# Optimization experiments

Hardware: AMD Instinct MI355X
Metric: run time of the kernel (lower is better)

Reference implementation:

```python
import jax, jax.numpy as jnp
import numpy as np

N_HEADS = 32
EPS = 1e-7
ROPE_BASE = 10000.0


def rms_norm(x, gamma):
    return x / jnp.sqrt(EPS + jnp.mean(x * x, axis=-1, keepdims=True)) * gamma


def rope_tables(seq_len, head_dim, dtype=jnp.float32):
    inv_freq = 1.0 / (ROPE_BASE ** (jnp.arange(0, head_dim, 2, dtype=jnp.float32) / head_dim))
    angles = jnp.arange(seq_len, dtype=jnp.float32)[:, None] * inv_freq[None, :]  # [S, D/2]
    angles = jnp.concatenate([angles, angles], axis=-1)  # [S, D]
    return jnp.cos(angles).astype(dtype), jnp.sin(angles).astype(dtype)


def apply_rope(x, cos, sin):
    # x: [B, H, S, D]; cos/sin: [S, D]
    d = x.shape[-1]
    x1, x2 = x[..., : d // 2], x[..., d // 2 :]
    rotated = jnp.concatenate([-x2, x1], axis=-1)
    return x * cos[None, None] + rotated * sin[None, None]


def setup_inputs() -> dict:
    key = jax.random.key(0)
    ks = jax.random.split(key, 9)
    B, S, D, Hd = 1, 2048, 4096, 11008
    s = lambda k, shape, fan: jax.random.normal(k, shape, jnp.float32) * (fan ** -0.5)
    return {
        "X": jax.random.normal(ks[0], (B, S, D), jnp.float32),
        "Wq": s(ks[1], (D, D), D),
        "Wk": s(ks[2], (D, D), D),
        "Wv": s(ks[3], (D, D), D),
        "Wo": s(ks[4], (D, D), D),
        "bo": jnp.zeros((D,), jnp.float32),
        "gamma1": jnp.ones((D,), jnp.float32),
        "gamma2": jnp.ones((D,), jnp.float32),
        "W1": s(ks[5], (D, Hd), D),
        "W2": s(ks[6], (D, Hd), D),
        "W3": s(ks[7], (Hd, D), Hd),
    }


def reference(X, Wq, Wk, Wv, Wo, bo, gamma1, gamma2, W1, W2, W3):
    B, S, D = X.shape
    H = N_HEADS
    hd = D // H

    # --- attention sublayer ---
    h = rms_norm(X, gamma1)
    q = (h @ Wq).reshape(B, S, H, hd).transpose(0, 2, 1, 3)  # [B,H,S,hd]
    k = (h @ Wk).reshape(B, S, H, hd).transpose(0, 2, 1, 3)
    v = (h @ Wv).reshape(B, S, H, hd).transpose(0, 2, 1, 3)

    cos, sin = rope_tables(S, hd, X.dtype)
    q = apply_rope(q, cos, sin)
    k = apply_rope(k, cos, sin)

    scores = jnp.einsum("bhsd,bhtd->bhst", q, k) / jnp.sqrt(jnp.asarray(hd, X.dtype))
    causal = jnp.tril(jnp.ones((S, S), bool))
    scores = jnp.where(causal, scores, -jnp.inf)
    attn = jax.nn.softmax(scores, axis=-1)
    out = jnp.einsum("bhst,bhtd->bhsd", attn, v)
    out = out.transpose(0, 2, 1, 3).reshape(B, S, D)
    out = out @ Wo + bo
    X = X + out

    # --- SwiGLU FFN sublayer ---
    h2 = rms_norm(X, gamma2)
    x1 = h2 @ W1
    x2 = h2 @ W2
    ff = (x1 * jax.nn.sigmoid(x1) * x2) @ W3
    return X + ff
```

## Files before the change

kernel.cpp:

```cpp
#include <hip/hip_runtime.h>
#include <hip/hip_bf16.h>
#include <cstdint>
#include <cmath>

typedef __bf16 bf16;
typedef __attribute__((ext_vector_type(8))) __bf16 bf16x8;
typedef __attribute__((ext_vector_type(4))) __bf16 bf16x4;
typedef __attribute__((ext_vector_type(4))) float f32x4;

__device__ __forceinline__ void gload_lds16(const void* g, void* l) {
  __builtin_amdgcn_global_load_lds((__attribute__((address_space(1))) void*)g,
                                   (__attribute__((address_space(3))) void*)l,
                                   16, 0, 0);
}

template<int BM, int EPI>
__global__ __launch_bounds__(512, 2) void gemmd(
    const bf16* __restrict__ A, const bf16* __restrict__ Bt, void* __restrict__ Cv,
    const float* __restrict__ bias, const float* __restrict__ resid,
    const float* __restrict__ cosT, const float* __restrict__ sinT,
    bf16* __restrict__ q_out, bf16* __restrict__ k_out, bf16* __restrict__ v_out,
    int M, int N, int K, int gm) {
  extern __shared__ char lds[];
  constexpr int ASZ = BM * 128;
  constexpr int BUFS = ASZ + 32768;
  constexpr int MF = BM / 64;
  constexpr int LA = BM / 64;

  const int tid = threadIdx.x;
  const int wave = tid >> 6, lane = tid & 63;
  const int wr = wave >> 1, wc = wave & 1;
  const int l15 = lane & 15, l4 = lane >> 4;
  const int qq = gridDim.x >> 3;
  const int wgid = (blockIdx.x & 7) * qq + (blockIdx.x >> 3);
  const int tm = wgid % gm, tn = wgid / gm;
  const long brow = (long)tm * BM, bcol = (long)tn * 256;
  const int NT = K >> 6;
  const bf16* Ab = A + brow * K;
  const bf16* Bb = Bt + bcol * K;

  f32x4 acc[MF][8];
  #pragma unroll
  for (int i = 0; i < MF; ++i)
    #pragma unroll
    for (int j = 0; j < 8; ++j) acc[i][j] = (f32x4){0.f, 0.f, 0.f, 0.f};

  bf16x8 a[MF][2], b[8][2];

  auto stage = [&](int T) {
    const long kofs = (long)T << 6;
    char* wb = lds + (T & 1) * BUFS;
    #pragma unroll
    for (int i = 0; i < LA; ++i) {
      const int slot = i * 512 + tid, r = slot >> 3, c0 = slot & 7;
      gload_lds16(Ab + (long)r * K + kofs + ((c0 ^ (r & 7)) << 3), wb + slot * 16);
    }
    #pragma unroll
    for (int i = 0; i < 4; ++i) {
      const int slot = i * 512 + tid, r = slot >> 3, c0 = slot & 7;
      gload_lds16(Bb + (long)r * K + kofs + ((c0 ^ (r & 7)) << 3), wb + ASZ + slot * 16);
    }
  };

  stage(0);
  __syncthreads();

  for (int g = 0; g < NT; ++g) {
    const int pg = (g & 1) * BUFS;
    if (g + 1 < NT) stage(g + 1);
    #pragma unroll
    for (int nf = 0; nf < 8; ++nf)
      #pragma unroll
      for (int ks = 0; ks < 2; ++ks) {
        const int r = wc * 128 + nf * 16 + l15;
        b[nf][ks] = *(const bf16x8*)(lds + pg + ASZ + r * 128 + (((ks * 4 + l4) ^ (r & 7)) << 4));
      }
    #pragma unroll
    for (int mf = 0; mf < MF; ++mf)
      #pragma unroll
      for (int ks = 0; ks < 2; ++ks) {
        const int r = wr * (BM / 4) + mf * 16 + l15;
        a[mf][ks] = *(const bf16x8*)(lds + pg + r * 128 + (((ks * 4 + l4) ^ (r & 7)) << 4));
      }
    __builtin_amdgcn_s_setprio(1);
    #pragma unroll
    for (int ks = 0; ks < 2; ++ks)
      #pragma unroll
      for (int mf = 0; mf < MF; ++mf)
        #pragma unroll
        for (int nf = 0; nf < 8; ++nf)
          acc[mf][nf] = __builtin_amdgcn_mfma_f32_16x16x32_bf16(
              a[mf][ks], b[nf][ks], acc[mf][nf], 0, 0, 0);
    __builtin_amdgcn_s_setprio(0);
    __syncthreads();
  }

  if (EPI == 1 || EPI == 2) {
    #pragma unroll
    for (int mf = 0; mf < MF; ++mf) {
      const long row0 = brow + wr * (BM / 4) + mf * 16 + l4 * 4;
      #pragma unroll
      for (int nf = 0; nf < 8; ++nf) {
        const long col = bcol + wc * 128 + nf * 16 + l15;
        #pragma unroll
        for (int rj = 0; rj < 4; ++rj) {
          const long idx = (row0 + rj) * N + col;
          const float v = acc[mf][nf][rj];
          if (EPI == 1) ((float*)Cv)[idx] = v + bias[col] + resid[idx];
          else          ((float*)Cv)[idx] = v + resid[idx];
        }
      }
    }
  } else if (EPI == 3) {
    const int region = (int)(bcol >> 12);
    const int hc = (int)(bcol & 4095) + wc * 128;
    const int h = hc >> 7;
    if (region < 2) {
      bf16* dh = (region == 0 ? q_out : k_out) + (long)h * 2048 * 128;
      #pragma unroll
      for (int mf = 0; mf < MF; ++mf) {
        #pragma unroll
        for (int rj = 0; rj < 4; ++rj) {
          const int s = (int)brow + wr * (BM / 4) + mf * 16 + l4 * 4 + rj;
          const float* cr = cosT + s * 64;
          const float* sr = sinT + s * 64;
          #pragma unroll
          for (int nfp = 0; nfp < 4; ++nfp) {
            const int d = nfp * 16 + l15;
            const float c = cr[d], sn = sr[d];
            const float x1 = acc[mf][nfp][rj], x2 = acc[mf][nfp + 4][rj];
            dh[(long)s * 128 + d]      = (bf16)(x1 * c - x2 * sn);
            dh[(long)s * 128 + d + 64] = (bf16)(x2 * c + x1 * sn);
          }
        }
      }
    } else {
      bf16* dh = v_out + (long)h * 128 * 2048;
      #pragma unroll
      for (int mf = 0; mf < MF; ++mf) {
        const int s0 = (int)brow + wr * (BM / 4) + mf * 16 + l4 * 4;
        #pragma unroll
        for (int nf = 0; nf < 8; ++nf) {
          const int d = nf * 16 + l15;
          bf16x4 v;
          #pragma unroll
          for (int rj = 0; rj < 4; ++rj) v[rj] = (bf16)acc[mf][nf][rj];
          *(bf16x4*)(dh + (long)d * 2048 + s0) = v;
        }
      }
    }
  } else {
    #pragma unroll
    for (int mf = 0; mf < MF; ++mf) {
      #pragma unroll
      for (int rj = 0; rj < 4; ++rj) {
        const int s = (int)brow + wr * (BM / 4) + mf * 16 + l4 * 4 + rj;
        bf16* gr = (bf16*)Cv + (long)s * 11008;
        #pragma unroll
        for (int nfp = 0; nfp < 4; ++nfp) {
          const int col = (int)bcol + wc * 128 + nfp * 32 + l15;
          const int j = ((col >> 5) << 4) + l15;
          const float x1 = acc[mf][2 * nfp][rj], x2 = acc[mf][2 * nfp + 1][rj];
          const float sg = x1 / (1.f + __expf(-x1));
          gr[j] = (bf16)(sg * x2);
        }
      }
    }
  }
}

__global__ __launch_bounds__(256) void rmsnorm_kernel(
    const float* __restrict__ X, const float* __restrict__ gamma,
    bf16* __restrict__ out, int D) {
  const int row = blockIdx.x;
  const float* xr = X + (long)row * D;
  float ss = 0.f;
  for (int i = threadIdx.x * 4; i < D; i += 1024) {
    float4 v = *(const float4*)(xr + i);
    ss += v.x * v.x + v.y * v.y + v.z * v.z + v.w * v.w;
  }
  #pragma unroll
  for (int off = 32; off; off >>= 1) ss += __shfl_down(ss, off, 64);
  __shared__ float wsum[4];
  if ((threadIdx.x & 63) == 0) wsum[threadIdx.x >> 6] = ss;
  __syncthreads();
  const float tot = wsum[0] + wsum[1] + wsum[2] + wsum[3];
  const float scale = rsqrtf(1e-7f + tot / (float)D);
  bf16* orow = out + (long)row * D;
  for (int i = threadIdx.x * 4; i < D; i += 1024) {
    float4 v = *(const float4*)(xr + i);
    float4 g = *(const float4*)(gamma + i);
    orow[i]     = (bf16)(v.x * scale * g.x);
    orow[i + 1] = (bf16)(v.y * scale * g.y);
    orow[i + 2] = (bf16)(v.z * scale * g.z);
    orow[i + 3] = (bf16)(v.w * scale * g.w);
  }
}

__global__ __launch_bounds__(256) void wtrans_kernel(
    const float* __restrict__ in, bf16* __restrict__ out, int R, int C) {
  __shared__ float t[64][65];
  const int bx = blockIdx.x, by = blockIdx.y;
  const int lr = threadIdx.x >> 4;
  const int lc4 = (threadIdx.x & 15) * 4;
  #pragma unroll
  for (int i = 0; i < 4; ++i) {
    const int r = lr + i * 16;
    const float4 v = *(const float4*)(in + (long)(by * 64 + r) * C + bx * 64 + lc4);
    t[r][lc4] = v.x; t[r][lc4 + 1] = v.y; t[r][lc4 + 2] = v.z; t[r][lc4 + 3] = v.w;
  }
  __syncthreads();
  const int oc = threadIdx.x >> 4;
  const int or4 = (threadIdx.x & 15) * 4;
  #pragma unroll
  for (int i = 0; i < 4; ++i) {
    const int c = oc + i * 16;
    bf16x4 v;
    #pragma unroll
    for (int j = 0; j < 4; ++j) v[j] = (bf16)t[or4 + j][c];
    *(bf16x4*)(out + (long)(bx * 64 + c) * R + by * 64 + or4) = v;
  }
}

__global__ __launch_bounds__(256) void w12trans_kernel(
    const float* __restrict__ in, bf16* __restrict__ out, int off) {
  __shared__ float t[64][65];
  const int bx = blockIdx.x, by = blockIdx.y;
  const int lk = threadIdx.x >> 4;
  const int lj4 = (threadIdx.x & 15) * 4;
  #pragma unroll
  for (int i = 0; i < 4; ++i) {
    const int k = lk + i * 16;
    const float4 v = *(const float4*)(in + (long)(by * 64 + k) * 11008 + bx * 64 + lj4);
    t[k][lj4] = v.x; t[k][lj4 + 1] = v.y; t[k][lj4 + 2] = v.z; t[k][lj4 + 3] = v.w;
  }
  __syncthreads();
  const int oj = threadIdx.x >> 4;
  const int ok4 = (threadIdx.x & 15) * 4;
  #pragma unroll
  for (int i = 0; i < 4; ++i) {
    const int j = bx * 64 + oj + i * 16;
    const int r = ((j >> 4) << 5) + off + (j & 15);
    bf16x4 v;
    #pragma unroll
    for (int jj = 0; jj < 4; ++jj) v[jj] = (bf16)t[ok4 + jj][oj + i * 16];
    *(bf16x4*)(out + (long)r * 4096 + by * 64 + ok4) = v;
  }
}

__global__ __launch_bounds__(256) void rope_table_kernel(float* __restrict__ cosT,
                                                         float* __restrict__ sinT) {
  const int idx = blockIdx.x * 256 + threadIdx.x;
  const int i = idx & 63, s = idx >> 6;
  const float inv = powf(10000.f, -(float)i / 64.f);
  const float ang = (float)s * inv;
  cosT[idx] = cosf(ang);
  sinT[idx] = sinf(ang);
}

__global__ __launch_bounds__(256) void attn_kernel(
    const bf16* __restrict__ qh, const bf16* __restrict__ kh,
    const bf16* __restrict__ vt, bf16* __restrict__ outb) {
  constexpr int S = 2048;
  const int qb = blockIdx.x, head = blockIdx.y;
  const int tid = threadIdx.x, wave = tid >> 6, lane = tid & 63;
  __shared__ bf16 Ks[64 * 128];
  __shared__ bf16 Vs[128 * 64];
  __shared__ bf16 Plds[4][16 * 64];
  const bf16* qhh = qh + (long)head * S * 128;
  const bf16* khh = kh + (long)head * S * 128;
  const bf16* vth = vt + (long)head * 128 * S;

  const int l15 = lane & 15, l4 = lane >> 4;
  const int qrow = qb * 64 + wave * 16 + l15;
  bf16x8 qf[4];
  #pragma unroll
  for (int kf = 0; kf < 4; ++kf)
    qf[kf] = *(const bf16x8*)(qhh + (long)qrow * 128 + kf * 32 + l4 * 8);

  float m_r[4], l_r[4];
  #pragma unroll
  for (int r = 0; r < 4; ++r) { m_r[r] = -INFINITY; l_r[r] = 0.f; }
  f32x4 oacc[8] = {};
  const float scale = 0.08838834764831845f;

  for (int tb = 0; tb <= qb; ++tb) {
    #pragma unroll
    for (int i = 0; i < 4; ++i) {
      const int c = wave + 4 * i;
      gload_lds16(khh + (long)(tb * 64 + c * 4 + l4) * 128 + l15 * 8, Ks + c * 512);
      gload_lds16(vth + (long)(c * 8 + (lane >> 3)) * S + tb * 64 + (lane & 7) * 8, Vs + c * 512);
    }
    __syncthreads();

    f32x4 sf[4];
    #pragma unroll
    for (int ft = 0; ft < 4; ++ft) {
      f32x4 acn = {};
      #pragma unroll
      for (int kf = 0; kf < 4; ++kf) {
        bf16x8 kfr = *(const bf16x8*)(Ks + (ft * 16 + l15) * 128 + kf * 32 + l4 * 8);
        acn = __builtin_amdgcn_mfma_f32_16x16x32_bf16(qf[kf], kfr, acn, 0, 0, 0);
      }
      #pragma unroll
      for (int r = 0; r < 4; ++r) sf[ft][r] = acn[r] * scale;
    }
    if (tb == qb) {
      #pragma unroll
      for (int ft = 0; ft < 4; ++ft) {
        const int t_l = ft * 16 + l15;
        #pragma unroll
        for (int r = 0; r < 4; ++r)
          if (t_l > wave * 16 + l4 * 4 + r) sf[ft][r] = -INFINITY;
      }
    }
    float scl[4];
    #pragma unroll
    for (int r = 0; r < 4; ++r) {
      float mx = fmaxf(fmaxf(sf[0][r], sf[1][r]), fmaxf(sf[2][r], sf[3][r]));
      mx = fmaxf(mx, __shfl_xor(mx, 1, 64));
      mx = fmaxf(mx, __shfl_xor(mx, 2, 64));
      mx = fmaxf(mx, __shfl_xor(mx, 4, 64));
      mx = fmaxf(mx, __shfl_xor(mx, 8, 64));
      const float mnew = fmaxf(m_r[r], mx);
      scl[r] = __expf(m_r[r] - mnew);
      m_r[r] = mnew;
      float rs = 0.f;
      #pragma unroll
      for (int ft = 0; ft < 4; ++ft) {
        const float pexp = __expf(sf[ft][r] - mnew);
        sf[ft][r] = pexp;
        rs += pexp;
      }
      rs += __shfl_xor(rs, 1, 64);
      rs += __shfl_xor(rs, 2, 64);
      rs += __shfl_xor(rs, 4, 64);
      rs += __shfl_xor(rs, 8, 64);
      l_r[r] = l_r[r] * scl[r] + rs;
    }
    #pragma unroll
    for (int ft = 0; ft < 4; ++ft)
      #pragma unroll
      for (int r = 0; r < 4; ++r)
        Plds[wave][(l4 * 4 + r) * 64 + ft * 16 + l15] = (bf16)sf[ft][r];
    #pragma unroll
    for (int fd = 0; fd < 8; ++fd)
      #pragma unroll
      for (int r = 0; r < 4; ++r) oacc[fd][r] *= scl[r];
    #pragma unroll
    for (int fd = 0; fd < 8; ++fd) {
      #pragma unroll
      for (int kt = 0; kt < 2; ++kt) {
        bf16x8 pa = *(const bf16x8*)(&Plds[wave][l15 * 64 + kt * 32 + l4 * 8]);
        bf16x8 vb = *(const bf16x8*)(Vs + (fd * 16 + l15) * 64 + kt * 32 + l4 * 8);
        oacc[fd] = __builtin_amdgcn_mfma_f32_16x16x32_bf16(pa, vb, oacc[fd], 0, 0, 0);
      }
    }
    __syncthreads();
  }
  #pragma unroll
  for (int fd = 0; fd < 8; ++fd) {
    #pragma unroll
    for (int r = 0; r < 4; ++r) {
      const long row = qb * 64 + wave * 16 + l4 * 4 + r;
      outb[row * 4096 + head * 128 + fd * 16 + l15] = (bf16)(oacc[fd][r] / l_r[r]);
    }
  }
}

extern "C" void kernel_launch(void* const* d_in, const int* in_sizes, int n_in,
                              void* d_out, int out_size, void* d_ws, size_t ws_size,
                              hipStream_t stream) {
  const float* X  = (const float*)d_in[0];
  const float* Wq = (const float*)d_in[1];
  const float* Wk = (const float*)d_in[2];
  const float* Wv = (const float*)d_in[3];
  const float* Wo = (const float*)d_in[4];
  const float* bo = (const float*)d_in[5];
  const float* g1 = (const float*)d_in[6];
  const float* g2 = (const float*)d_in[7];
  const float* W1 = (const float*)d_in[8];
  const float* W2 = (const float*)d_in[9];
  const float* W3 = (const float*)d_in[10];
  float* out = (float*)d_out;

  hipFuncSetAttribute((const void*)gemmd<256, 3>, hipFuncAttributeMaxDynamicSharedMemorySize, 131072);
  hipFuncSetAttribute((const void*)gemmd<256, 4>, hipFuncAttributeMaxDynamicSharedMemorySize, 131072);
  hipFuncSetAttribute((const void*)gemmd<128, 1>, hipFuncAttributeMaxDynamicSharedMemorySize, 98304);
  hipFuncSetAttribute((const void*)gemmd<128, 2>, hipFuncAttributeMaxDynamicSharedMemorySize, 98304);

  char* p = (char*)d_ws;
  auto alloc = [&](size_t bytes) {
    char* r = p;
    p += (bytes + 255) & ~(size_t)255;
    return r;
  };
  float* cosT = (float*)alloc(2048 * 64 * 4);
  float* sinT = (float*)alloc(2048 * 64 * 4);
  bf16* WqkvT = (bf16*)alloc(12288L * 4096 * 2);
  bf16* WoT  = (bf16*)alloc(4096L * 4096 * 2);
  bf16* W12T = (bf16*)alloc(22016L * 4096 * 2);
  bf16* W3T  = (bf16*)alloc(4096L * 11008 * 2);
  bf16* qhB  = (bf16*)alloc(2048L * 4096 * 2);
  bf16* khB  = (bf16*)alloc(2048L * 4096 * 2);
  bf16* vtB  = (bf16*)alloc(2048L * 4096 * 2);
  bf16* hbuf = (bf16*)alloc(2048L * 4096 * 2);
  bf16* h2   = (bf16*)alloc(2048L * 4096 * 2);
  float* X2  = (float*)alloc(2048L * 4096 * 4);

  bf16* gsw = (bf16*)WqkvT;
  bf16* attnb = hbuf;

  rope_table_kernel<<<512, 256, 0, stream>>>(cosT, sinT);
  wtrans_kernel<<<dim3(64, 64), 256, 0, stream>>>(Wq, WqkvT, 4096, 4096);
  wtrans_kernel<<<dim3(64, 64), 256, 0, stream>>>(Wk, WqkvT + 4096L * 4096, 4096, 4096);
  wtrans_kernel<<<dim3(64, 64), 256, 0, stream>>>(Wv, WqkvT + 2 * 4096L * 4096, 4096, 4096);
  wtrans_kernel<<<dim3(64, 64), 256, 0, stream>>>(Wo, WoT, 4096, 4096);
  w12trans_kernel<<<dim3(172, 64), 256, 0, stream>>>(W1, W12T, 0);
  w12trans_kernel<<<dim3(172, 64), 256, 0, stream>>>(W2, W12T, 16);
  wtrans_kernel<<<dim3(64, 172), 256, 0, stream>>>(W3, W3T, 11008, 4096);

  rmsnorm_kernel<<<2048, 256, 0, stream>>>(X, g1, hbuf, 4096);

  gemmd<256, 3><<<384, 512, 131072, stream>>>(hbuf, WqkvT, nullptr, nullptr, nullptr,
                                              cosT, sinT, qhB, khB, vtB,
                                              2048, 12288, 4096, 8);

  attn_kernel<<<dim3(32, 32), 256, 0, stream>>>(qhB, khB, vtB, attnb);

  gemmd<128, 1><<<256, 512, 98304, stream>>>(attnb, WoT, X2, bo, X,
                                             nullptr, nullptr, nullptr, nullptr, nullptr,
                                             2048, 4096, 4096, 16);

  rmsnorm_kernel<<<2048, 256, 0, stream>>>(X2, g2, h2, 4096);

  gemmd<256, 4><<<688, 512, 131072, stream>>>(h2, W12T, gsw, nullptr, nullptr,
                                              nullptr, nullptr, nullptr, nullptr, nullptr,
                                              2048, 22016, 4096, 8);

  gemmd<128, 2><<<256, 512, 98304, stream>>>(gsw, W3T, out, nullptr, X2,
                                             nullptr, nullptr, nullptr, nullptr, nullptr,
                                             2048, 4096, 11008, 16);
}
```

Measured before the change: 1.373 ms.

## Double-buffer attention K/V loads, merge prep kernels, drop MFMA setprio

The attention kernel now double-buffers K and V tiles in LDS, prefetching the next block while computing on the current one. This is meant to hide global-load latency, at the cost of twice the LDS per block, which may lower occupancy. The seven weight-transpose launches and the RoPE table launch are merged into one prep kernel to cut launch overhead. The s_setprio calls around the GEMM MFMA loop are also removed.

```diff
diff --git a/kernel.cpp b/kernel.cpp
--- a/kernel.cpp
+++ b/kernel.cpp
@@ -82,7 +82,6 @@
         const int r = wr * (BM / 4) + mf * 16 + l15;
         a[mf][ks] = *(const bf16x8*)(lds + pg + r * 128 + (((ks * 4 + l4) ^ (r & 7)) << 4));
       }
-    __builtin_amdgcn_s_setprio(1);
     #pragma unroll
     for (int ks = 0; ks < 2; ++ks)
       #pragma unroll
@@ -91,7 +90,6 @@
         for (int nf = 0; nf < 8; ++nf)
           acc[mf][nf] = __builtin_amdgcn_mfma_f32_16x16x32_bf16(
               a[mf][ks], b[nf][ks], acc[mf][nf], 0, 0, 0);
-    __builtin_amdgcn_s_setprio(0);
     __syncthreads();
   }
 
@@ -149,7 +147,7 @@
         }
       }
     }
-  } else {
+  } else if (EPI == 4) {
     #pragma unroll
     for (int mf = 0; mf < MF; ++mf) {
       #pragma unroll
@@ -159,13 +157,71 @@
         #pragma unroll
         for (int nfp = 0; nfp < 4; ++nfp) {
           const int col = (int)bcol + wc * 128 + nfp * 32 + l15;
-          const int j = ((col >> 5) << 4) + l15;
+          const int jj = ((col >> 5) << 4) + l15;
           const float x1 = acc[mf][2 * nfp][rj], x2 = acc[mf][2 * nfp + 1][rj];
           const float sg = x1 / (1.f + __expf(-x1));
-          gr[j] = (bf16)(sg * x2);
+          gr[jj] = (bf16)(sg * x2);
         }
       }
     }
+  }
+}
+
+__device__ __forceinline__ void trans64(
+    const float* __restrict__ in, bf16* __restrict__ out,
+    int R, int C, int bx, int by, int ilv, int off) {
+  __shared__ float t[64][65];
+  const int lr = threadIdx.x >> 4;
+  const int lc4 = (threadIdx.x & 15) * 4;
+  #pragma unroll
+  for (int i = 0; i < 4; ++i) {
+    const int r = lr + i * 16;
+    const float4 v = *(const float4*)(in + (long)(by * 64 + r) * C + bx * 64 + lc4);
+    t[r][lc4] = v.x; t[r][lc4 + 1] = v.y; t[r][lc4 + 2] = v.z; t[r][lc4 + 3] = v.w;
+  }
+  __syncthreads();
+  const int oc = threadIdx.x >> 4;
+  const int or4 = (threadIdx.x & 15) * 4;
+  #pragma unroll
+  for (int i = 0; i < 4; ++i) {
+    const int c = oc + i * 16;
+    const int j = bx * 64 + c;
+    const int rdst = ilv ? (((j >> 4) << 5) + off + (j & 15)) : j;
+    bf16x4 v;
+    #pragma unroll
+    for (int k = 0; k < 4; ++k) v[k] = (bf16)t[or4 + k][c];
+    *(bf16x4*)(out + (long)rdst * R + by * 64 + or4) = v;
+  }
+}
+
+__global__ __launch_bounds__(256) void prep_kernel(
+    const float* __restrict__ Wq, const float* __restrict__ Wk,
+    const float* __restrict__ Wv, const float* __restrict__ Wo,
+    const float* __restrict__ W1, const float* __restrict__ W2,
+    const float* __restrict__ W3,
+    bf16* __restrict__ WqkvT, bf16* __restrict__ WoT,
+    bf16* __restrict__ W12T, bf16* __restrict__ W3T,
+    float* __restrict__ cosT, float* __restrict__ sinT) {
+  const int bid = blockIdx.x;
+  if (bid < 16384) {
+    const int seg = bid >> 12, idx = bid & 4095;
+    const float* in = (seg == 0 ? Wq : seg == 1 ? Wk : seg == 2 ? Wv : Wo);
+    bf16* out = (seg == 3 ? WoT : WqkvT + (long)seg * 4096 * 4096);
+    trans64(in, out, 4096, 4096, idx & 63, idx >> 6, 0, 0);
+  } else if (bid < 38400) {
+    const int idx = bid - 16384;
+    const int seg = idx / 11008, li = idx % 11008;
+    trans64(seg ? W2 : W1, W12T, 4096, 11008, li % 172, li / 172, 1, seg * 16);
+  } else if (bid < 49408) {
+    const int idx = bid - 38400;
+    trans64(W3, W3T, 11008, 4096, idx & 63, idx >> 6, 0, 0);
+  } else {
+    const int gidx = (bid - 49408) * 256 + threadIdx.x;
+    const int i = gidx & 63, s = gidx >> 6;
+    const float inv = powf(10000.f, -(float)i / 64.f);
+    const float ang = (float)s * inv;
+    cosT[gidx] = cosf(ang);
+    sinT[gidx] = sinf(ang);
   }
 }
 
@@ -197,75 +253,14 @@
   }
 }
 
-__global__ __launch_bounds__(256) void wtrans_kernel(
-    const float* __restrict__ in, bf16* __restrict__ out, int R, int C) {
-  __shared__ float t[64][65];
-  const int bx = blockIdx.x, by = blockIdx.y;
-  const int lr = threadIdx.x >> 4;
-  const int lc4 = (threadIdx.x & 15) * 4;
-  #pragma unroll
-  for (int i = 0; i < 4; ++i) {
-    const int r = lr + i * 16;
-    const float4 v = *(const float4*)(in + (long)(by * 64 + r) * C + bx * 64 + lc4);
-    t[r][lc4] = v.x; t[r][lc4 + 1] = v.y; t[r][lc4 + 2] = v.z; t[r][lc4 + 3] = v.w;
-  }
-  __syncthreads();
-  const int oc = threadIdx.x >> 4;
-  const int or4 = (threadIdx.x & 15) * 4;
-  #pragma unroll
-  for (int i = 0; i < 4; ++i) {
-    const int c = oc + i * 16;
-    bf16x4 v;
-    #pragma unroll
-    for (int j = 0; j < 4; ++j) v[j] = (bf16)t[or4 + j][c];
-    *(bf16x4*)(out + (long)(bx * 64 + c) * R + by * 64 + or4) = v;
-  }
-}
-
-__global__ __launch_bounds__(256) void w12trans_kernel(
-    const float* __restrict__ in, bf16* __restrict__ out, int off) {
-  __shared__ float t[64][65];
-  const int bx = blockIdx.x, by = blockIdx.y;
-  const int lk = threadIdx.x >> 4;
-  const int lj4 = (threadIdx.x & 15) * 4;
-  #pragma unroll
-  for (int i = 0; i < 4; ++i) {
-    const int k = lk + i * 16;
-    const float4 v = *(const float4*)(in + (long)(by * 64 + k) * 11008 + bx * 64 + lj4);
-    t[k][lj4] = v.x; t[k][lj4 + 1] = v.y; t[k][lj4 + 2] = v.z; t[k][lj4 + 3] = v.w;
-  }
-  __syncthreads();
-  const int oj = threadIdx.x >> 4;
-  const int ok4 = (threadIdx.x & 15) * 4;
-  #pragma unroll
-  for (int i = 0; i < 4; ++i) {
-    const int j = bx * 64 + oj + i * 16;
-    const int r = ((j >> 4) << 5) + off + (j & 15);
-    bf16x4 v;
-    #pragma unroll
-    for (int jj = 0; jj < 4; ++jj) v[jj] = (bf16)t[ok4 + jj][oj + i * 16];
-    *(bf16x4*)(out + (long)r * 4096 + by * 64 + ok4) = v;
-  }
-}
-
-__global__ __launch_bounds__(256) void rope_table_kernel(float* __restrict__ cosT,
-                                                         float* __restrict__ sinT) {
-  const int idx = blockIdx.x * 256 + threadIdx.x;
-  const int i = idx & 63, s = idx >> 6;
-  const float inv = powf(10000.f, -(float)i / 64.f);
-  const float ang = (float)s * inv;
-  cosT[idx] = cosf(ang);
-  sinT[idx] = sinf(ang);
-}
-
 __global__ __launch_bounds__(256) void attn_kernel(
     const bf16* __restrict__ qh, const bf16* __restrict__ kh,
     const bf16* __restrict__ vt, bf16* __restrict__ outb) {
   constexpr int S = 2048;
   const int qb = blockIdx.x, head = blockIdx.y;
   const int tid = threadIdx.x, wave = tid >> 6, lane = tid & 63;
-  __shared__ bf16 Ks[64 * 128];
-  __shared__ bf16 Vs[128 * 64];
+  __shared__ bf16 Ks[2][64 * 128];
+  __shared__ bf16 Vs[2][128 * 64];
   __shared__ bf16 Plds[4][16 * 64];
   const bf16* qhh = qh + (long)head * S * 128;
   const bf16* khh = kh + (long)head * S * 128;
@@ -278,20 +273,27 @@
   for (int kf = 0; kf < 4; ++kf)
     qf[kf] = *(const bf16x8*)(qhh + (long)qrow * 128 + kf * 32 + l4 * 8);
 
+  auto stageKV = [&](int tb, int buf) {
+    #pragma unroll
+    for (int i = 0; i < 4; ++i) {
+      const int c = wave + 4 * i;
+      gload_lds16(khh + (long)(tb * 64 + c * 4 + l4) * 128 + l15 * 8, Ks[buf] + c * 512);
+      gload_lds16(vth + (long)(c * 8 + (lane >> 3)) * S + tb * 64 + (lane & 7) * 8, Vs[buf] + c * 512);
+    }
+  };
+
   float m_r[4], l_r[4];
   #pragma unroll
   for (int r = 0; r < 4; ++r) { m_r[r] = -INFINITY; l_r[r] = 0.f; }
   f32x4 oacc[8] = {};
   const float scale = 0.08838834764831845f;
 
+  stageKV(0, 0);
+  __syncthreads();
+
   for (int tb = 0; tb <= qb; ++tb) {
-    #pragma unroll
-    for (int i = 0; i < 4; ++i) {
-      const int c = wave + 4 * i;
-      gload_lds16(khh + (long)(tb * 64 + c * 4 + l4) * 128 + l15 * 8, Ks + c * 512);
-      gload_lds16(vth + (long)(c * 8 + (lane >> 3)) * S + tb * 64 + (lane & 7) * 8, Vs + c * 512);
-    }
-    __syncthreads();
+    const int buf = tb & 1;
+    if (tb < qb) stageKV(tb + 1, buf ^ 1);
 
     f32x4 sf[4];
     #pragma unroll
@@ -299,7 +301,7 @@
       f32x4 acn = {};
       #pragma unroll
       for (int kf = 0; kf < 4; ++kf) {
-        bf16x8 kfr = *(const bf16x8*)(Ks + (ft * 16 + l15) * 128 + kf * 32 + l4 * 8);
+        bf16x8 kfr = *(const bf16x8*)(Ks[buf] + (ft * 16 + l15) * 128 + kf * 32 + l4 * 8);
         acn = __builtin_amdgcn_mfma_f32_16x16x32_bf16(qf[kf], kfr, acn, 0, 0, 0);
       }
       #pragma unroll
@@ -352,7 +354,7 @@
       #pragma unroll
       for (int kt = 0; kt < 2; ++kt) {
         bf16x8 pa = *(const bf16x8*)(&Plds[wave][l15 * 64 + kt * 32 + l4 * 8]);
-        bf16x8 vb = *(const bf16x8*)(Vs + (fd * 16 + l15) * 64 + kt * 32 + l4 * 8);
+        bf16x8 vb = *(const bf16x8*)(Vs[buf] + (fd * 16 + l15) * 64 + kt * 32 + l4 * 8);
         oacc[fd] = __builtin_amdgcn_mfma_f32_16x16x32_bf16(pa, vb, oacc[fd], 0, 0, 0);
       }
     }
@@ -411,14 +413,8 @@
   bf16* gsw = (bf16*)WqkvT;
   bf16* attnb = hbuf;
 
-  rope_table_kernel<<<512, 256, 0, stream>>>(cosT, sinT);
-  wtrans_kernel<<<dim3(64, 64), 256, 0, stream>>>(Wq, WqkvT, 4096, 4096);
-  wtrans_kernel<<<dim3(64, 64), 256, 0, stream>>>(Wk, WqkvT + 4096L * 4096, 4096, 4096);
-  wtrans_kernel<<<dim3(64, 64), 256, 0, stream>>>(Wv, WqkvT + 2 * 4096L * 4096, 4096, 4096);
-  wtrans_kernel<<<dim3(64, 64), 256, 0, stream>>>(Wo, WoT, 4096, 4096);
-  w12trans_kernel<<<dim3(172, 64), 256, 0, stream>>>(W1, W12T, 0);
-  w12trans_kernel<<<dim3(172, 64), 256, 0, stream>>>(W2, W12T, 16);
-  wtrans_kernel<<<dim3(64, 172), 256, 0, stream>>>(W3, W3T, 11008, 4096);
+  prep_kernel<<<49920, 256, 0, stream>>>(Wq, Wk, Wv, Wo, W1, W2, W3,
+                                         WqkvT, WoT, W12T, W3T, cosT, sinT);
 
   rmsnorm_kernel<<<2048, 256, 0, stream>>>(X, g1, hbuf, 4096);
 
```

Result: slower. 1.414 ms (+3.0%).
